# Performance work log

Hardware: AMD Instinct MI355X
Metric: run time of the kernel (lower is better)

Reference implementation:

```python
import jax, jax.numpy as jnp
import numpy as np
from jax import lax

HORIZON = 333.0
LAM = 0.95
DISCOUNT = 1.0 - 1.0 / HORIZON  # contdisc=False

B, T, D, H = 1024, 65, 512, 512


def _mlp(x, W1, b1, W2, b2, W3, b3):
    # x: [B, T, D] -> scalar critic mean per step [B, T]
    h = jax.nn.silu(jnp.einsum('btd,dh->bth', x, W1) + b1)
    h = jax.nn.silu(jnp.einsum('bth,hk->btk', h, W2) + b2)
    out = jnp.einsum('bth,ho->bto', h, W3) + b3
    return out[..., 0]


def setup_inputs() -> dict:
    key = jax.random.key(0)
    ks = jax.random.split(key, 8)
    s = 1.0 / np.sqrt(D)
    sh = 1.0 / np.sqrt(H)
    return {
        'feat': jax.random.normal(ks[0], (B, T, D), jnp.float32),
        'reward': jax.random.normal(ks[1], (B, T), jnp.float32) * 0.1,
        'cont': jnp.ones((B, T), jnp.float32),
        'voffset': jnp.zeros((1,), jnp.float32),
        'vscale': jnp.ones((1,), jnp.float32),
        'W1n': jax.random.normal(ks[2], (D, H), jnp.float32) * s,
        'b1n': jnp.zeros((H,), jnp.float32),
        'W2n': jax.random.normal(ks[3], (H, H), jnp.float32) * sh,
        'b2n': jnp.zeros((H,), jnp.float32),
        'W3n': jax.random.normal(ks[4], (H, 1), jnp.float32) * sh,
        'b3n': jnp.zeros((1,), jnp.float32),
        'W1s': jax.random.normal(ks[5], (D, H), jnp.float32) * s,
        'b1s': jnp.zeros((H,), jnp.float32),
        'W2s': jax.random.normal(ks[6], (H, H), jnp.float32) * sh,
        'b2s': jnp.zeros((H,), jnp.float32),
        'W3s': jax.random.normal(ks[7], (H, 1), jnp.float32) * sh,
        'b3s': jnp.zeros((1,), jnp.float32),
    }


def reference(feat, reward, cont, voffset, vscale,
              W1n, b1n, W2n, b2n, W3n, b3n,
              W1s, b1s, W2s, b2s, W3s, b3s):
    critic = _mlp(feat, W1n, b1n, W2n, b2n, W3n, b3n)        # [B, T]
    slowcritic = _mlp(feat, W1s, b1s, W2s, b2s, W3s, b3s)    # [B, T]
    val = critic * vscale + voffset
    slowval = slowcritic * vscale + voffset
    tarval = slowval  # config.agent.slowtar = True

    disc = cont[:, 1:] * DISCOUNT                             # [B, T-1]
    interm = reward[:, 1:] + (1.0 - LAM) * disc * tarval[:, 1:]
    boot = tarval[:, -1]                                      # [B]

    # reversed linear recurrence r_t = interm_t + disc_t*lam*r_{t+1}
    xs = (jnp.moveaxis(interm, 1, 0), jnp.moveaxis(disc, 1, 0))  # [T-1, B]

    def step(carry, x):
        i_t, d_t = x
        r = i_t + d_t * LAM * carry
        return r, r

    _, ys = lax.scan(step, boot, xs, reverse=True)            # [T-1, B], time order t=0..T-2
    ret = jnp.moveaxis(ys, 0, 1)                              # [B, T-1]
    return ret
```

## Files before the change

kernel.cpp:

```cpp
#include <hip/hip_runtime.h>
#include <stdint.h>


#define MROWS 66560
#define RBLK 520
#define LAMF 0.95f
#define DISCF ((float)(1.0 - 1.0 / 333.0))

typedef __attribute__((ext_vector_type(8))) __bf16 bf16x8;
typedef __attribute__((ext_vector_type(4))) float f32x4;
typedef __attribute__((ext_vector_type(4))) unsigned int u32x4;

__device__ __forceinline__ unsigned short f2bf(float f) {
  unsigned int u = __float_as_uint(f);
  return (unsigned short)((u + 0x7FFFu + ((u >> 16) & 1u)) >> 16);
}
__device__ __forceinline__ float silu_f(float x) { return x / (1.0f + __expf(-x)); }

__device__ __forceinline__ void gload_lds16(const void* g, void* l) {
  __builtin_amdgcn_global_load_lds(
      (const __attribute__((address_space(1))) void*)g,
      (__attribute__((address_space(3))) void*)l, 16, 0, 0);
}

__global__ __launch_bounds__(256) void prep_kernel(
    const float* __restrict__ W1, const float* __restrict__ W2,
    unsigned short* __restrict__ Wt1, unsigned short* __restrict__ Wt2,
    float* __restrict__ tarval) {
  int b = blockIdx.x;
  if (b < 128) {
    const float* W = (b < 64) ? W1 : W2;
    unsigned short* Wt = (b < 64) ? Wt1 : Wt2;
    int tb = b & 63;
    int tk = (tb >> 3) * 64;
    int tn = (tb & 7) * 64;
    __shared__ float tile[64][65];
    int tx = threadIdx.x & 63;
    int ty4 = threadIdx.x >> 6;
#pragma unroll
    for (int i = 0; i < 16; ++i) {
      int row = ty4 * 16 + i;
      tile[row][tx] = W[(size_t)(tk + row) * 512 + tn + tx];
    }
    __syncthreads();
#pragma unroll
    for (int i = 0; i < 16; ++i) {
      int nrow = ty4 * 16 + i;
      Wt[(size_t)(tn + nrow) * 512 + tk + tx] = f2bf(tile[tx][nrow]);
    }
  } else {
    int id = (b - 128) * 256 + threadIdx.x;
#pragma unroll
    for (int i = 0; i < 17; ++i) {
      int idx = id + i * 4096;
      if (idx < MROWS) tarval[idx] = 0.0f;
    }
  }
}

__device__ __forceinline__ void tile_map(int bid, int& rb, int& cb) {
  int xcd = bid & 7;
  int idx = bid >> 3;
  rb = xcd * 65 + (idx >> 2);
  cb = idx & 3;
}

__global__ __launch_bounds__(256) void gemm1_kernel(
    const float* __restrict__ A, const unsigned short* __restrict__ Bt,
    const float* __restrict__ bias, unsigned short* __restrict__ Hout) {
  __shared__ __align__(16) unsigned char lds[65536];

  int rb, cb; tile_map(blockIdx.x, rb, cb);
  const int m0 = rb * 128, n0 = cb * 128;
  const int tid = threadIdx.x;
  const int lane = tid & 63, w = tid >> 6;
  const int wr = w >> 1, wc = w & 1;
  const int q = lane >> 4, r = lane & 15;

  f32x4 acc[4][4] = {};
  f32x4 pa[8];

  {
#pragma unroll
    for (int i = 0; i < 4; ++i) {
      int L = (i * 256 + tid) * 16;
      int row = L >> 7, kb = L & 127;
      const float* src = A + (size_t)(m0 + row) * 512 + (kb >> 1);
      pa[2 * i]     = *(const f32x4*)(src);
      pa[2 * i + 1] = *(const f32x4*)(src + 4);
    }
    unsigned char* Bl = lds + 16384;
    const int base = w * 1024;
#pragma unroll
    for (int i = 0; i < 4; ++i) {
      int L = i * 4096 + base + lane * 16;
      int row = L >> 7, kb = L & 127;
      gload_lds16((const void*)(Bt + (size_t)(n0 + row) * 512 + (kb >> 1)),
                  (void*)(Bl + i * 4096 + base));
    }
    unsigned char* Al = lds;
#pragma unroll
    for (int i = 0; i < 4; ++i) {
      int L = (i * 256 + tid) * 16;
      union { unsigned short h[8]; u32x4 u; } p;
      p.h[0] = f2bf(pa[2*i][0]); p.h[1] = f2bf(pa[2*i][1]);
      p.h[2] = f2bf(pa[2*i][2]); p.h[3] = f2bf(pa[2*i][3]);
      p.h[4] = f2bf(pa[2*i+1][0]); p.h[5] = f2bf(pa[2*i+1][1]);
      p.h[6] = f2bf(pa[2*i+1][2]); p.h[7] = f2bf(pa[2*i+1][3]);
      *(u32x4*)(Al + L) = p.u;
    }
  }
  __syncthreads();

#pragma unroll
  for (int t = 0; t < 8; ++t) {
    unsigned char* Acur = lds + (t & 1) * 32768;
    unsigned char* Bcur = Acur + 16384;
    unsigned char* Anx  = lds + ((t + 1) & 1) * 32768;
    unsigned char* Bnx  = Anx + 16384;

    if (t < 7) {
      const int ks = (t + 1) * 64;
#pragma unroll
      for (int i = 0; i < 4; ++i) {
        int L = (i * 256 + tid) * 16;
        int row = L >> 7, kb = L & 127;
        const float* src = A + (size_t)(m0 + row) * 512 + ks + (kb >> 1);
        pa[2 * i]     = *(const f32x4*)(src);
        pa[2 * i + 1] = *(const f32x4*)(src + 4);
      }
      const int base = w * 1024;
#pragma unroll
      for (int i = 0; i < 4; ++i) {
        int L = i * 4096 + base + lane * 16;
        int row = L >> 7, kb = L & 127;
        gload_lds16((const void*)(Bt + (size_t)(n0 + row) * 512 + ks + (kb >> 1)),
                    (void*)(Bnx + i * 4096 + base));
      }
    }

#pragma unroll
    for (int kk = 0; kk < 2; ++kk) {
      bf16x8 af[4], bfr[4];
      const int kbyte = kk * 64 + q * 16;
#pragma unroll
      for (int m = 0; m < 4; ++m)
        af[m] = *(const bf16x8*)(Acur + (wr * 64 + m * 16 + r) * 128 + kbyte);
#pragma unroll
      for (int n = 0; n < 4; ++n)
        bfr[n] = *(const bf16x8*)(Bcur + (wc * 64 + n * 16 + r) * 128 + kbyte);
#pragma unroll
      for (int m = 0; m < 4; ++m)
#pragma unroll
        for (int n = 0; n < 4; ++n)
          acc[m][n] = __builtin_amdgcn_mfma_f32_16x16x32_bf16(af[m], bfr[n], acc[m][n], 0, 0, 0);
    }

    if (t < 7) {
#pragma unroll
      for (int i = 0; i < 4; ++i) {
        int L = (i * 256 + tid) * 16;
        union { unsigned short h[8]; u32x4 u; } p;
        p.h[0] = f2bf(pa[2*i][0]); p.h[1] = f2bf(pa[2*i][1]);
        p.h[2] = f2bf(pa[2*i][2]); p.h[3] = f2bf(pa[2*i][3]);
        p.h[4] = f2bf(pa[2*i+1][0]); p.h[5] = f2bf(pa[2*i+1][1]);
        p.h[6] = f2bf(pa[2*i+1][2]); p.h[7] = f2bf(pa[2*i+1][3]);
        *(u32x4*)(Anx + L) = p.u;
      }
    }
    __syncthreads();
  }

#pragma unroll
  for (int n = 0; n < 4; ++n) {
    const int col = n0 + wc * 64 + n * 16 + r;
    const float bn = bias[col];
#pragma unroll
    for (int m = 0; m < 4; ++m) {
      const int rbase = m0 + wr * 64 + m * 16 + q * 4;
#pragma unroll
      for (int i = 0; i < 4; ++i)
        Hout[(size_t)(rbase + i) * 512 + col] = f2bf(silu_f(acc[m][n][i] + bn));
    }
  }
}

__global__ __launch_bounds__(256) void gemm2_kernel(
    const unsigned short* __restrict__ A, const unsigned short* __restrict__ Bt,
    const float* __restrict__ bias, const float* __restrict__ W3,
    float* __restrict__ tarval) {
  __shared__ __align__(16) unsigned char lds[65536];

  int rb, cb; tile_map(blockIdx.x, rb, cb);
  const int m0 = rb * 128, n0 = cb * 128;
  const int tid = threadIdx.x;
  const int lane = tid & 63, w = tid >> 6;
  const int wr = w >> 1, wc = w & 1;
  const int q = lane >> 4, r = lane & 15;

  f32x4 acc[4][4] = {};
  const int base = w * 1024;

  {
    unsigned char* Al = lds;
    unsigned char* Bl = lds + 16384;
#pragma unroll
    for (int i = 0; i < 4; ++i) {
      int L = i * 4096 + base + lane * 16;
      int row = L >> 7, kb = L & 127;
      gload_lds16((const void*)(A + (size_t)(m0 + row) * 512 + (kb >> 1)),
                  (void*)(Al + i * 4096 + base));
      gload_lds16((const void*)(Bt + (size_t)(n0 + row) * 512 + (kb >> 1)),
                  (void*)(Bl + i * 4096 + base));
    }
  }
  __syncthreads();

#pragma unroll
  for (int t = 0; t < 8; ++t) {
    unsigned char* Acur = lds + (t & 1) * 32768;
    unsigned char* Bcur = Acur + 16384;
    unsigned char* Anx  = lds + ((t + 1) & 1) * 32768;
    unsigned char* Bnx  = Anx + 16384;

    if (t < 7) {
      const int ks = (t + 1) * 64;
#pragma unroll
      for (int i = 0; i < 4; ++i) {
        int L = i * 4096 + base + lane * 16;
        int row = L >> 7, kb = L & 127;
        gload_lds16((const void*)(A + (size_t)(m0 + row) * 512 + ks + (kb >> 1)),
                    (void*)(Anx + i * 4096 + base));
        gload_lds16((const void*)(Bt + (size_t)(n0 + row) * 512 + ks + (kb >> 1)),
                    (void*)(Bnx + i * 4096 + base));
      }
    }

#pragma unroll
    for (int kk = 0; kk < 2; ++kk) {
      bf16x8 af[4], bfr[4];
      const int kbyte = kk * 64 + q * 16;
#pragma unroll
      for (int m = 0; m < 4; ++m)
        af[m] = *(const bf16x8*)(Acur + (wr * 64 + m * 16 + r) * 128 + kbyte);
#pragma unroll
      for (int n = 0; n < 4; ++n)
        bfr[n] = *(const bf16x8*)(Bcur + (wc * 64 + n * 16 + r) * 128 + kbyte);
#pragma unroll
      for (int m = 0; m < 4; ++m)
#pragma unroll
        for (int n = 0; n < 4; ++n)
          acc[m][n] = __builtin_amdgcn_mfma_f32_16x16x32_bf16(af[m], bfr[n], acc[m][n], 0, 0, 0);
    }
    __syncthreads();
  }

#pragma unroll
  for (int m = 0; m < 4; ++m) {
    float ps0 = 0.f, ps1 = 0.f, ps2 = 0.f, ps3 = 0.f;
#pragma unroll
    for (int n = 0; n < 4; ++n) {
      const int col = n0 + wc * 64 + n * 16 + r;
      const float bn = bias[col];
      const float w3 = W3[col];
      ps0 += silu_f(acc[m][n][0] + bn) * w3;
      ps1 += silu_f(acc[m][n][1] + bn) * w3;
      ps2 += silu_f(acc[m][n][2] + bn) * w3;
      ps3 += silu_f(acc[m][n][3] + bn) * w3;
    }
    float ps[4] = {ps0, ps1, ps2, ps3};
#pragma unroll
    for (int i = 0; i < 4; ++i) {
      float v = ps[i];
      v += __shfl_xor(v, 1);
      v += __shfl_xor(v, 2);
      v += __shfl_xor(v, 4);
      v += __shfl_xor(v, 8);
      if (r == 0) {
        int row = m0 + wr * 64 + m * 16 + q * 4 + i;
        atomicAdd(&tarval[row], v);
      }
    }
  }
}

__global__ __launch_bounds__(64) void scan_kernel(
    const float* __restrict__ tarval, const float* __restrict__ reward,
    const float* __restrict__ cont, const float* __restrict__ voffset,
    const float* __restrict__ vscale, const float* __restrict__ b3,
    float* __restrict__ out) {
  __shared__ float tv[64];
  __shared__ float ret[64];
  const int b = blockIdx.x, t = threadIdx.x;
  tv[t] = (tarval[b * 65 + 1 + t] + b3[0]) * vscale[0] + voffset[0];
  __syncthreads();
  if (t == 0) {
    float carry = tv[63];
    for (int j = 63; j >= 0; --j) {
      const int tt = j + 1;
      const float disc = cont[b * 65 + tt] * DISCF;
      const float r = reward[b * 65 + tt] + disc * ((1.0f - LAMF) * tv[j] + LAMF * carry);
      ret[j] = r;
      carry = r;
    }
  }
  __syncthreads();
  out[b * 64 + t] = ret[t];
}

extern "C" void kernel_launch(void* const* d_in, const int* in_sizes, int n_in,
                              void* d_out, int out_size, void* d_ws, size_t ws_size,
                              hipStream_t stream) {
  const float* feat    = (const float*)d_in[0];
  const float* reward  = (const float*)d_in[1];
  const float* cont    = (const float*)d_in[2];
  const float* voffset = (const float*)d_in[3];
  const float* vscale  = (const float*)d_in[4];
  const float* W1s = (const float*)d_in[11];
  const float* b1s = (const float*)d_in[12];
  const float* W2s = (const float*)d_in[13];
  const float* b2s = (const float*)d_in[14];
  const float* W3s = (const float*)d_in[15];
  const float* b3s = (const float*)d_in[16];

  char* ws = (char*)d_ws;
  unsigned short* Wt1 = (unsigned short*)ws;
  unsigned short* Wt2 = (unsigned short*)(ws + (512u << 10));
  float* tarval       = (float*)(ws + (1024u << 10));
  unsigned short* H1  = (unsigned short*)(ws + (2048u << 10));

  prep_kernel<<<144, 256, 0, stream>>>(W1s, W2s, Wt1, Wt2, tarval);
  gemm1_kernel<<<RBLK * 4, 256, 0, stream>>>(feat, Wt1, b1s, H1);
  gemm2_kernel<<<RBLK * 4, 256, 0, stream>>>(H1, Wt2, b2s, W3s, tarval);
  scan_kernel<<<1024, 64, 0, stream>>>(tarval, reward, cont, voffset, vscale, b3s,
                                       (float*)d_out);
}
```

Measured before the change: 375.8 us.

## XOR-swizzle LDS tiles and deepen GEMM prefetch with manual waitcnt barriers

Both GEMM kernels now store LDS tiles with an XOR swizzle on the 16-byte column chunk, which avoids bank conflicts on the MFMA fragment reads. The B operand (and A in gemm2) is prefetched two K-steps ahead with direct global-to-LDS loads. Plain __syncthreads is replaced by explicit s_waitcnt vmcnt/lgkmcnt plus s_barrier, and all fragments are read into registers before the buffer is refilled. This exposes more memory latency overlap and removes LDS conflicts, but it depends on hand-counted vmcnt values that must match the issued loads exactly.

```diff
diff --git a/kernel.cpp b/kernel.cpp
--- a/kernel.cpp
+++ b/kernel.cpp
@@ -21,6 +21,13 @@
   __builtin_amdgcn_global_load_lds(
       (const __attribute__((address_space(1))) void*)g,
       (__attribute__((address_space(3))) void*)l, 16, 0, 0);
+}
+
+__device__ __forceinline__ u32x4 pack8(const f32x4& a, const f32x4& b) {
+  union { unsigned short h[8]; u32x4 u; } p;
+  p.h[0] = f2bf(a[0]); p.h[1] = f2bf(a[1]); p.h[2] = f2bf(a[2]); p.h[3] = f2bf(a[3]);
+  p.h[4] = f2bf(b[0]); p.h[5] = f2bf(b[1]); p.h[6] = f2bf(b[2]); p.h[7] = f2bf(b[3]);
+  return p.u;
 }
 
 __global__ __launch_bounds__(256) void prep_kernel(
@@ -76,99 +83,94 @@
   const int lane = tid & 63, w = tid >> 6;
   const int wr = w >> 1, wc = w & 1;
   const int q = lane >> 4, r = lane & 15;
+  const unsigned int rx = (unsigned)(r & 7) << 4;
 
   f32x4 acc[4][4] = {};
   f32x4 pa[8];
 
-  {
-#pragma unroll
-    for (int i = 0; i < 4; ++i) {
-      int L = (i * 256 + tid) * 16;
-      int row = L >> 7, kb = L & 127;
-      const float* src = A + (size_t)(m0 + row) * 512 + (kb >> 1);
-      pa[2 * i]     = *(const f32x4*)(src);
-      pa[2 * i + 1] = *(const f32x4*)(src + 4);
-    }
-    unsigned char* Bl = lds + 16384;
-    const int base = w * 1024;
-#pragma unroll
-    for (int i = 0; i < 4; ++i) {
-      int L = i * 4096 + base + lane * 16;
-      int row = L >> 7, kb = L & 127;
-      gload_lds16((const void*)(Bt + (size_t)(n0 + row) * 512 + (kb >> 1)),
-                  (void*)(Bl + i * 4096 + base));
-    }
-    unsigned char* Al = lds;
-#pragma unroll
-    for (int i = 0; i < 4; ++i) {
-      int L = (i * 256 + tid) * 16;
-      union { unsigned short h[8]; u32x4 u; } p;
-      p.h[0] = f2bf(pa[2*i][0]); p.h[1] = f2bf(pa[2*i][1]);
-      p.h[2] = f2bf(pa[2*i][2]); p.h[3] = f2bf(pa[2*i][3]);
-      p.h[4] = f2bf(pa[2*i+1][0]); p.h[5] = f2bf(pa[2*i+1][1]);
-      p.h[6] = f2bf(pa[2*i+1][2]); p.h[7] = f2bf(pa[2*i+1][3]);
-      *(u32x4*)(Al + L) = p.u;
-    }
-  }
-  __syncthreads();
+  const int a_row_off = tid >> 3;
+  const int a_col = (tid & 7) * 8;
+  const unsigned int awx = ((unsigned)((tid >> 3) & 7)) << 4;
+  const int b_row_off = w * 8 + (lane >> 3);
+  const int b_col = ((lane & 7) ^ (lane >> 3)) * 8;
+
+#pragma unroll
+  for (int i = 0; i < 4; ++i) {
+    const float* s = A + (size_t)(m0 + i * 32 + a_row_off) * 512 + a_col;
+    pa[2 * i] = *(const f32x4*)s; pa[2 * i + 1] = *(const f32x4*)(s + 4);
+  }
+#pragma unroll
+  for (int i = 0; i < 4; ++i)
+    gload_lds16(Bt + (size_t)(n0 + i * 32 + b_row_off) * 512 + b_col,
+                lds + 16384 + i * 4096 + w * 1024);
+#pragma unroll
+  for (int i = 0; i < 4; ++i)
+    gload_lds16(Bt + (size_t)(n0 + i * 32 + b_row_off) * 512 + 64 + b_col,
+                lds + 49152 + i * 4096 + w * 1024);
+#pragma unroll
+  for (int i = 0; i < 4; ++i)
+    *(u32x4*)(lds + ((unsigned)(i * 4096 + tid * 16) ^ awx)) =
+        pack8(pa[2 * i], pa[2 * i + 1]);
 
 #pragma unroll
   for (int t = 0; t < 8; ++t) {
+    if (t < 7) asm volatile("s_waitcnt vmcnt(4) lgkmcnt(0)" ::: "memory");
+    else       asm volatile("s_waitcnt vmcnt(0) lgkmcnt(0)" ::: "memory");
+    __builtin_amdgcn_s_barrier();
+
     unsigned char* Acur = lds + (t & 1) * 32768;
     unsigned char* Bcur = Acur + 16384;
-    unsigned char* Anx  = lds + ((t + 1) & 1) * 32768;
-    unsigned char* Bnx  = Anx + 16384;
 
     if (t < 7) {
       const int ks = (t + 1) * 64;
 #pragma unroll
       for (int i = 0; i < 4; ++i) {
-        int L = (i * 256 + tid) * 16;
-        int row = L >> 7, kb = L & 127;
-        const float* src = A + (size_t)(m0 + row) * 512 + ks + (kb >> 1);
-        pa[2 * i]     = *(const f32x4*)(src);
-        pa[2 * i + 1] = *(const f32x4*)(src + 4);
-      }
-      const int base = w * 1024;
-#pragma unroll
-      for (int i = 0; i < 4; ++i) {
-        int L = i * 4096 + base + lane * 16;
-        int row = L >> 7, kb = L & 127;
-        gload_lds16((const void*)(Bt + (size_t)(n0 + row) * 512 + ks + (kb >> 1)),
-                    (void*)(Bnx + i * 4096 + base));
-      }
-    }
-
+        const float* s = A + (size_t)(m0 + i * 32 + a_row_off) * 512 + ks + a_col;
+        pa[2 * i] = *(const f32x4*)s; pa[2 * i + 1] = *(const f32x4*)(s + 4);
+      }
+    }
+
+    bf16x8 af[2][4], bfr[2][4];
 #pragma unroll
     for (int kk = 0; kk < 2; ++kk) {
-      bf16x8 af[4], bfr[4];
-      const int kbyte = kk * 64 + q * 16;
+      const unsigned int kb = kk * 64 + q * 16;
+#pragma unroll
+      for (int m = 0; m < 4; ++m) {
+        const unsigned int row = wr * 64 + m * 16 + r;
+        af[kk][m] = *(const bf16x8*)(Acur + ((row * 128 + kb) ^ rx));
+      }
+#pragma unroll
+      for (int n = 0; n < 4; ++n) {
+        const unsigned int row = wc * 64 + n * 16 + r;
+        bfr[kk][n] = *(const bf16x8*)(Bcur + ((row * 128 + kb) ^ rx));
+      }
+    }
+    asm volatile("s_waitcnt lgkmcnt(0)" ::: "memory");
+    __builtin_amdgcn_sched_barrier(0);
+    __builtin_amdgcn_s_barrier();
+
+    if (t + 2 < 8) {
+      const int ks = (t + 2) * 64;
+#pragma unroll
+      for (int i = 0; i < 4; ++i)
+        gload_lds16(Bt + (size_t)(n0 + i * 32 + b_row_off) * 512 + ks + b_col,
+                    Bcur + i * 4096 + w * 1024);
+    }
+    if (t < 7) {
+      unsigned char* Anx = lds + ((t + 1) & 1) * 32768;
+#pragma unroll
+      for (int i = 0; i < 4; ++i)
+        *(u32x4*)(Anx + ((unsigned)(i * 4096 + tid * 16) ^ awx)) =
+            pack8(pa[2 * i], pa[2 * i + 1]);
+    }
+
+#pragma unroll
+    for (int kk = 0; kk < 2; ++kk)
 #pragma unroll
       for (int m = 0; m < 4; ++m)
-        af[m] = *(const bf16x8*)(Acur + (wr * 64 + m * 16 + r) * 128 + kbyte);
-#pragma unroll
-      for (int n = 0; n < 4; ++n)
-        bfr[n] = *(const bf16x8*)(Bcur + (wc * 64 + n * 16 + r) * 128 + kbyte);
-#pragma unroll
-      for (int m = 0; m < 4; ++m)
 #pragma unroll
         for (int n = 0; n < 4; ++n)
-          acc[m][n] = __builtin_amdgcn_mfma_f32_16x16x32_bf16(af[m], bfr[n], acc[m][n], 0, 0, 0);
-    }
-
-    if (t < 7) {
-#pragma unroll
-      for (int i = 0; i < 4; ++i) {
-        int L = (i * 256 + tid) * 16;
-        union { unsigned short h[8]; u32x4 u; } p;
-        p.h[0] = f2bf(pa[2*i][0]); p.h[1] = f2bf(pa[2*i][1]);
-        p.h[2] = f2bf(pa[2*i][2]); p.h[3] = f2bf(pa[2*i][3]);
-        p.h[4] = f2bf(pa[2*i+1][0]); p.h[5] = f2bf(pa[2*i+1][1]);
-        p.h[6] = f2bf(pa[2*i+1][2]); p.h[7] = f2bf(pa[2*i+1][3]);
-        *(u32x4*)(Anx + L) = p.u;
-      }
-    }
-    __syncthreads();
+          acc[m][n] = __builtin_amdgcn_mfma_f32_16x16x32_bf16(af[kk][m], bfr[kk][n], acc[m][n], 0, 0, 0);
   }
 
 #pragma unroll
@@ -197,62 +199,73 @@
   const int lane = tid & 63, w = tid >> 6;
   const int wr = w >> 1, wc = w & 1;
   const int q = lane >> 4, r = lane & 15;
+  const unsigned int rx = (unsigned)(r & 7) << 4;
 
   f32x4 acc[4][4] = {};
-  const int base = w * 1024;
-
-  {
-    unsigned char* Al = lds;
-    unsigned char* Bl = lds + 16384;
-#pragma unroll
-    for (int i = 0; i < 4; ++i) {
-      int L = i * 4096 + base + lane * 16;
-      int row = L >> 7, kb = L & 127;
-      gload_lds16((const void*)(A + (size_t)(m0 + row) * 512 + (kb >> 1)),
-                  (void*)(Al + i * 4096 + base));
-      gload_lds16((const void*)(Bt + (size_t)(n0 + row) * 512 + (kb >> 1)),
-                  (void*)(Bl + i * 4096 + base));
-    }
-  }
-  __syncthreads();
+  const int s_row_off = w * 8 + (lane >> 3);
+  const int s_col = ((lane & 7) ^ (lane >> 3)) * 8;
+
+#pragma unroll
+  for (int i = 0; i < 4; ++i) {
+    gload_lds16(A  + (size_t)(m0 + i * 32 + s_row_off) * 512 + s_col,
+                lds + i * 4096 + w * 1024);
+    gload_lds16(Bt + (size_t)(n0 + i * 32 + s_row_off) * 512 + s_col,
+                lds + 16384 + i * 4096 + w * 1024);
+  }
+#pragma unroll
+  for (int i = 0; i < 4; ++i) {
+    gload_lds16(A  + (size_t)(m0 + i * 32 + s_row_off) * 512 + 64 + s_col,
+                lds + 32768 + i * 4096 + w * 1024);
+    gload_lds16(Bt + (size_t)(n0 + i * 32 + s_row_off) * 512 + 64 + s_col,
+                lds + 49152 + i * 4096 + w * 1024);
+  }
 
 #pragma unroll
   for (int t = 0; t < 8; ++t) {
+    if (t < 7) asm volatile("s_waitcnt vmcnt(8) lgkmcnt(0)" ::: "memory");
+    else       asm volatile("s_waitcnt vmcnt(0) lgkmcnt(0)" ::: "memory");
+    __builtin_amdgcn_s_barrier();
+
     unsigned char* Acur = lds + (t & 1) * 32768;
     unsigned char* Bcur = Acur + 16384;
-    unsigned char* Anx  = lds + ((t + 1) & 1) * 32768;
-    unsigned char* Bnx  = Anx + 16384;
-
-    if (t < 7) {
-      const int ks = (t + 1) * 64;
+
+    bf16x8 af[2][4], bfr[2][4];
+#pragma unroll
+    for (int kk = 0; kk < 2; ++kk) {
+      const unsigned int kb = kk * 64 + q * 16;
+#pragma unroll
+      for (int m = 0; m < 4; ++m) {
+        const unsigned int row = wr * 64 + m * 16 + r;
+        af[kk][m] = *(const bf16x8*)(Acur + ((row * 128 + kb) ^ rx));
+      }
+#pragma unroll
+      for (int n = 0; n < 4; ++n) {
+        const unsigned int row = wc * 64 + n * 16 + r;
+        bfr[kk][n] = *(const bf16x8*)(Bcur + ((row * 128 + kb) ^ rx));
+      }
+    }
+    asm volatile("s_waitcnt lgkmcnt(0)" ::: "memory");
+    __builtin_amdgcn_sched_barrier(0);
+    __builtin_amdgcn_s_barrier();
+
+    if (t + 2 < 8) {
+      const int ks = (t + 2) * 64;
 #pragma unroll
       for (int i = 0; i < 4; ++i) {
-        int L = i * 4096 + base + lane * 16;
-        int row = L >> 7, kb = L & 127;
-        gload_lds16((const void*)(A + (size_t)(m0 + row) * 512 + ks + (kb >> 1)),
-                    (void*)(Anx + i * 4096 + base));
-        gload_lds16((const void*)(Bt + (size_t)(n0 + row) * 512 + ks + (kb >> 1)),
-                    (void*)(Bnx + i * 4096 + base));
-      }
-    }
-
-#pragma unroll
-    for (int kk = 0; kk < 2; ++kk) {
-      bf16x8 af[4], bfr[4];
-      const int kbyte = kk * 64 + q * 16;
+        gload_lds16(A  + (size_t)(m0 + i * 32 + s_row_off) * 512 + ks + s_col,
+                    Acur + i * 4096 + w * 1024);
+        gload_lds16(Bt + (size_t)(n0 + i * 32 + s_row_off) * 512 + ks + s_col,
+                    Bcur + i * 4096 + w * 1024);
+      }
+    }
+
+#pragma unroll
+    for (int kk = 0; kk < 2; ++kk)
 #pragma unroll
       for (int m = 0; m < 4; ++m)
-        af[m] = *(const bf16x8*)(Acur + (wr * 64 + m * 16 + r) * 128 + kbyte);
-#pragma unroll
-      for (int n = 0; n < 4; ++n)
-        bfr[n] = *(const bf16x8*)(Bcur + (wc * 64 + n * 16 + r) * 128 + kbyte);
-#pragma unroll
-      for (int m = 0; m < 4; ++m)
 #pragma unroll
         for (int n = 0; n < 4; ++n)
-          acc[m][n] = __builtin_amdgcn_mfma_f32_16x16x32_bf16(af[m], bfr[n], acc[m][n], 0, 0, 0);
-    }
-    __syncthreads();
+          acc[m][n] = __builtin_amdgcn_mfma_f32_16x16x32_bf16(af[kk][m], bfr[kk][n], acc[m][n], 0, 0, 0);
   }
 
 #pragma unroll
```

Result: faster. 343.0 us (-8.7%).
